# Kernel tuning notes

Measured on AMD Instinct MI355X. Metric: run time of the kernel, lower is better.

The kernel has to match this reference:

```python
import jax, jax.numpy as jnp
import numpy as np

N = 256  # node_num, fully-connected graph
NEG_SLOPE = 0.2


def _edges(n):
    # fully-connected permutations; PyG GATConv removes then re-adds self-loops,
    # so effectively all n*n (src, dst) pairs are present.
    idx = jnp.arange(n)
    src = jnp.repeat(idx, n)
    dst = jnp.tile(idx, n)
    return src, dst


def _gat_conv(x, W, att_src, att_dst, b, src, dst, n):
    # x: [N, Fin], W: [Fin, H*C], att_*: [H, C], b: [H*C]
    H, C = att_src.shape
    h = (x @ W).reshape(n, H, C)                       # [N, H, C]
    a_src = jnp.einsum('nhc,hc->nh', h, att_src)       # [N, H]
    a_dst = jnp.einsum('nhc,hc->nh', h, att_dst)
    e = jax.nn.leaky_relu(a_src[src] + a_dst[dst], NEG_SLOPE)  # [E, H]
    # segment softmax over incoming edges of each dst node
    m = jax.ops.segment_max(e, dst, num_segments=n)    # [N, H]
    p = jnp.exp(e - m[dst])
    denom = jax.ops.segment_sum(p, dst, num_segments=n)
    alpha = p / (denom[dst] + 1e-16)                   # [E, H]
    msg = h[src] * alpha[:, :, None]                   # [E, H, C]
    out = jax.ops.segment_sum(msg, dst, num_segments=n)  # [N, H, C]
    return out.reshape(n, H * C) + b


def setup_inputs() -> dict:
    key = jax.random.key(0)
    ks = jax.random.split(key, 7)
    Fin, H1, C1 = 128, 4, 128
    s = lambda fan: 1.0 / np.sqrt(fan)
    return {
        'x': jax.random.normal(ks[0], (8, N, Fin), dtype=jnp.float32),
        'W1': jax.random.normal(ks[1], (Fin, H1 * C1), dtype=jnp.float32) * s(Fin),
        'att_src1': jax.random.normal(ks[2], (H1, C1), dtype=jnp.float32) * s(C1),
        'att_dst1': jax.random.normal(ks[3], (H1, C1), dtype=jnp.float32) * s(C1),
        'b1': jnp.zeros((H1 * C1,), dtype=jnp.float32),
        'W2': jax.random.normal(ks[4], (H1 * C1, Fin), dtype=jnp.float32) * s(H1 * C1),
        'att_src2': jax.random.normal(ks[5], (1, Fin), dtype=jnp.float32) * s(Fin),
        'att_dst2': jax.random.normal(ks[6], (1, Fin), dtype=jnp.float32) * s(Fin),
        'b2': jnp.zeros((Fin,), dtype=jnp.float32),
    }


def reference(x, W1, att_src1, att_dst1, b1, W2, att_src2, att_dst2, b2):
    src, dst = _edges(N)

    def one_graph(xi):
        h = jax.nn.relu(_gat_conv(xi, W1, att_src1, att_dst1, b1, src, dst, N))
        return _gat_conv(h, W2, att_src2, att_dst2, b2, src, dst, N)

    return jax.vmap(one_graph)(x)  # [B, N, Fin]
```

## Files before the change

kernel.cpp:

```cpp
#include <hip/hip_runtime.h>
#include <hip/hip_bf16.h>

#define BATCH 8
#define NN    256
#define FIN   128
#define H1    4
#define C1    128
#define HC1   512
#define NEG_SLOPE 0.2f

__device__ __forceinline__ float lrelu(float v) {
    return v > 0.f ? v : NEG_SLOPE * v;
}

__global__ __launch_bounds__(512, 4)
void gemm1_fused(const float* __restrict__ x, const float* __restrict__ W1,
                 const float* __restrict__ as1, const float* __restrict__ ad1,
                 float* __restrict__ h1, float* __restrict__ a_src,
                 float* __restrict__ a_dst) {
    __shared__ float xs[4][FIN];
    __shared__ float redS[4][8], redD[4][8];
    const int b = blockIdx.y, r0 = blockIdx.x * 4, t = threadIdx.x;

    if (t < 128)
        ((float4*)xs)[t] = ((const float4*)(x + (size_t)(b * NN + r0) * FIN))[t];
    __syncthreads();

    float a0 = 0.f, a1 = 0.f, a2 = 0.f, a3 = 0.f;
    #pragma unroll 8
    for (int k = 0; k < FIN; ++k) {
        float w = W1[k * HC1 + t];
        a0 = fmaf(xs[0][k], w, a0);
        a1 = fmaf(xs[1][k], w, a1);
        a2 = fmaf(xs[2][k], w, a2);
        a3 = fmaf(xs[3][k], w, a3);
    }
    float acc[4] = {a0, a1, a2, a3};
    #pragma unroll
    for (int r = 0; r < 4; ++r)
        h1[(b * NN + r0 + r) * HC1 + t] = acc[r];

    const float as = as1[t], ad = ad1[t];
    const int w = t >> 6, lane = t & 63;
    #pragma unroll
    for (int r = 0; r < 4; ++r) {
        float s = acc[r] * as, d = acc[r] * ad;
        #pragma unroll
        for (int off = 32; off > 0; off >>= 1) {
            s += __shfl_down(s, off, 64);
            d += __shfl_down(d, off, 64);
        }
        if (lane == 0) { redS[r][w] = s; redD[r][w] = d; }
    }
    __syncthreads();
    if (t < 16) {
        int r = t & 3, h = t >> 2;
        a_src[(b * NN + r0 + r) * H1 + h] = redS[r][2 * h] + redS[r][2 * h + 1];
        a_dst[(b * NN + r0 + r) * H1 + h] = redD[r][2 * h] + redD[r][2 * h + 1];
    }
}

__global__ __launch_bounds__(512, 4)
void agg1_kernel(const float* __restrict__ h1, const float* __restrict__ a_src,
                 const float* __restrict__ a_dst, const float* __restrict__ b1,
                 float* __restrict__ hrelu) {
    __shared__ float s_as[NN];
    __shared__ float s_ad[16];
    __shared__ float sp[16][NN];
    __shared__ float s_den[16];

    const int b = blockIdx.z, head = blockIdx.y, d0 = blockIdx.x * 16;
    const int t = threadIdx.x;

    if (t < NN) s_as[t] = a_src[(b * NN + t) * H1 + head];
    if (t < 16) s_ad[t] = a_dst[(b * NN + d0 + t) * H1 + head];
    __syncthreads();

    const int d = t >> 5, l = t & 31;
    const float adst = s_ad[d];
    float e[8];
    float mx = -1e30f;
    #pragma unroll
    for (int i = 0; i < 8; ++i) {
        float v = lrelu(s_as[l + i * 32] + adst);
        e[i] = v;
        mx = fmaxf(mx, v);
    }
    #pragma unroll
    for (int off = 16; off > 0; off >>= 1)
        mx = fmaxf(mx, __shfl_down(mx, off, 32));
    mx = __shfl(mx, 0, 32);
    float sum = 0.f;
    #pragma unroll
    for (int i = 0; i < 8; ++i) {
        float p = __expf(e[i] - mx);
        sp[d][l + i * 32] = p;
        sum += p;
    }
    #pragma unroll
    for (int off = 16; off > 0; off >>= 1)
        sum += __shfl_down(sum, off, 32);
    if (l == 0) s_den[d] = sum + 1e-16f;
    __syncthreads();

    const int c = t & 127, g = t >> 7;
    float c0 = 0.f, c1 = 0.f, c2 = 0.f, c3 = 0.f;
    const float* hb = h1 + (size_t)(b * NN) * HC1 + head * C1 + c;
    #pragma unroll 4
    for (int src = 0; src < NN; ++src) {
        float hv = hb[(size_t)src * HC1];
        c0 = fmaf(sp[g * 4 + 0][src], hv, c0);
        c1 = fmaf(sp[g * 4 + 1][src], hv, c1);
        c2 = fmaf(sp[g * 4 + 2][src], hv, c2);
        c3 = fmaf(sp[g * 4 + 3][src], hv, c3);
    }
    float accs[4] = {c0, c1, c2, c3};
    const float bias = b1[head * C1 + c];
    #pragma unroll
    for (int j = 0; j < 4; ++j) {
        int dst = d0 + g * 4 + j;
        float v = accs[j] / s_den[g * 4 + j] + bias;
        hrelu[(b * NN + dst) * HC1 + head * C1 + c] = fmaxf(v, 0.f);
    }
}

__global__ __launch_bounds__(512, 4)
void gemm2_fused(const float* __restrict__ hrelu, const float* __restrict__ W2,
                 const float* __restrict__ as2, const float* __restrict__ ad2,
                 float* __restrict__ h2, float* __restrict__ a_src,
                 float* __restrict__ a_dst) {
    __shared__ float xs[4][HC1];
    __shared__ float red[3][4][FIN];
    __shared__ float redS[4][2], redD[4][2];
    const int b = blockIdx.y, r0 = blockIdx.x * 4, t = threadIdx.x;

    ((float4*)xs)[t] = ((const float4*)(hrelu + (size_t)(b * NN + r0) * HC1))[t];
    __syncthreads();

    const int c = t & 127, g = t >> 7;
    float acc[4] = {0.f, 0.f, 0.f, 0.f};
    const int k0 = g * 128;
    #pragma unroll 8
    for (int kk = 0; kk < 128; ++kk) {
        int k = k0 + kk;
        float w = W2[k * FIN + c];
        acc[0] = fmaf(xs[0][k], w, acc[0]);
        acc[1] = fmaf(xs[1][k], w, acc[1]);
        acc[2] = fmaf(xs[2][k], w, acc[2]);
        acc[3] = fmaf(xs[3][k], w, acc[3]);
    }
    if (g > 0) {
        #pragma unroll
        for (int r = 0; r < 4; ++r) red[g - 1][r][c] = acc[r];
    }
    __syncthreads();
    if (g == 0) {
        #pragma unroll
        for (int r = 0; r < 4; ++r) {
            acc[r] += red[0][r][c] + red[1][r][c] + red[2][r][c];
            h2[(b * NN + r0 + r) * FIN + c] = acc[r];
        }
        const int lane = t & 63, w2 = t >> 6;
        const float as = as2[c], ad = ad2[c];
        #pragma unroll
        for (int r = 0; r < 4; ++r) {
            float s = acc[r] * as, d = acc[r] * ad;
            #pragma unroll
            for (int off = 32; off > 0; off >>= 1) {
                s += __shfl_down(s, off, 64);
                d += __shfl_down(d, off, 64);
            }
            if (lane == 0) { redS[r][w2] = s; redD[r][w2] = d; }
        }
    }
    __syncthreads();
    if (t < 4) {
        a_src[b * NN + r0 + t] = redS[t][0] + redS[t][1];
        a_dst[b * NN + r0 + t] = redD[t][0] + redD[t][1];
    }
}

__global__ __launch_bounds__(512, 4)
void agg2_kernel(const float* __restrict__ h2, const float* __restrict__ a_src,
                 const float* __restrict__ a_dst, const float* __restrict__ b2,
                 float* __restrict__ out) {
    __shared__ float s_as[NN];
    __shared__ float s_ad[4];
    __shared__ float sp[4][NN];
    __shared__ float redm[4][2], reds[4][2];
    __shared__ float s_den[4];
    __shared__ float redA[3][4][FIN];

    const int b = blockIdx.y, d0 = blockIdx.x * 4, t = threadIdx.x;

    if (t < NN) s_as[t] = a_src[b * NN + t];
    if (t < 4) s_ad[t] = a_dst[b * NN + d0 + t];
    __syncthreads();

    const int d = t >> 7, l = t & 127, lane = t & 63, w = (t >> 6) & 1;
    const float adst = s_ad[d];
    float e0 = lrelu(s_as[l] + adst);
    float e1 = lrelu(s_as[l + 128] + adst);
    float mx = fmaxf(e0, e1);
    #pragma unroll
    for (int off = 32; off > 0; off >>= 1)
        mx = fmaxf(mx, __shfl_down(mx, off, 64));
    if (lane == 0) redm[d][w] = mx;
    __syncthreads();
    const float m = fmaxf(redm[d][0], redm[d][1]);
    float p0 = __expf(e0 - m), p1 = __expf(e1 - m);
    sp[d][l] = p0;
    sp[d][l + 128] = p1;
    float sum = p0 + p1;
    #pragma unroll
    for (int off = 32; off > 0; off >>= 1)
        sum += __shfl_down(sum, off, 64);
    if (lane == 0) reds[d][w] = sum;
    __syncthreads();
    if (t < 4) s_den[t] = reds[t][0] + reds[t][1] + 1e-16f;
    __syncthreads();

    const int c = l, q = d;
    float a4[4] = {0.f, 0.f, 0.f, 0.f};
    const float* hb = h2 + ((size_t)(b * NN) + q * 64) * FIN + c;
    #pragma unroll 8
    for (int i = 0; i < 64; ++i) {
        float hv = hb[(size_t)i * FIN];
        int src = q * 64 + i;
        a4[0] = fmaf(sp[0][src], hv, a4[0]);
        a4[1] = fmaf(sp[1][src], hv, a4[1]);
        a4[2] = fmaf(sp[2][src], hv, a4[2]);
        a4[3] = fmaf(sp[3][src], hv, a4[3]);
    }
    if (q > 0) {
        #pragma unroll
        for (int j = 0; j < 4; ++j) redA[q - 1][j][c] = a4[j];
    }
    __syncthreads();
    if (q == 0) {
        #pragma unroll
        for (int j = 0; j < 4; ++j) {
            float v = a4[j] + redA[0][j][c] + redA[1][j][c] + redA[2][j][c];
            out[(b * NN + d0 + j) * FIN + c] = v / s_den[j] + b2[c];
        }
    }
}

extern "C" void kernel_launch(void* const* d_in, const int* in_sizes, int n_in,
                              void* d_out, int out_size, void* d_ws, size_t ws_size,
                              hipStream_t stream) {
    const float* x   = (const float*)d_in[0];
    const float* W1  = (const float*)d_in[1];
    const float* as1 = (const float*)d_in[2];
    const float* ad1 = (const float*)d_in[3];
    const float* b1  = (const float*)d_in[4];
    const float* W2  = (const float*)d_in[5];
    const float* as2 = (const float*)d_in[6];
    const float* ad2 = (const float*)d_in[7];
    const float* b2  = (const float*)d_in[8];
    float* out = (float*)d_out;

    float* ws = (float*)d_ws;
    float* h1     = ws;
    float* hrelu  = ws + 1048576;
    float* h2     = ws + 2097152;
    float* a_src1 = ws + 2359296;
    float* a_dst1 = ws + 2367488;
    float* a_src2 = ws + 2375680;
    float* a_dst2 = ws + 2377728;

    gemm1_fused<<<dim3(64, BATCH), 512, 0, stream>>>(x, W1, as1, ad1, h1, a_src1, a_dst1);
    agg1_kernel<<<dim3(16, H1, BATCH), 512, 0, stream>>>(h1, a_src1, a_dst1, b1, hrelu);
    gemm2_fused<<<dim3(64, BATCH), 512, 0, stream>>>(hrelu, W2, as2, ad2, h2, a_src2, a_dst2);
    agg2_kernel<<<dim3(64, BATCH), 512, 0, stream>>>(h2, a_src2, a_dst2, b2, out);
}
```

Before: 122.7 us.

## Register-tile gemm1 with float4 outputs and transpose softmax weights for vector LDS reads

gemm1 now has each thread compute a 4x4 output tile from 16-row blocks of x, loading W1 as float4 and cutting the grid to 256 threads per block. This raises reuse of the W1 loads, which is meant to reduce global memory traffic. The attention-weight buffers in both aggregation kernels are stored transposed (src-major), so one float4 LDS read supplies all four destinations per step. gemm2 reads x from shared memory as float4. The trade-off is fewer blocks in gemm1, which may leave the GPU underoccupied, and extra padding in shared memory.

Result: slower. 129.1 us (+5.2%).

```diff
diff --git a/kernel.cpp b/kernel.cpp
--- a/kernel.cpp
+++ b/kernel.cpp
@@ -12,51 +12,89 @@
 __device__ __forceinline__ float lrelu(float v) {
     return v > 0.f ? v : NEG_SLOPE * v;
 }
-
-__global__ __launch_bounds__(512, 4)
+__device__ __forceinline__ float4 f4fma(float s, float4 w, float4 a) {
+    a.x = fmaf(s, w.x, a.x); a.y = fmaf(s, w.y, a.y);
+    a.z = fmaf(s, w.z, a.z); a.w = fmaf(s, w.w, a.w);
+    return a;
+}
+
+__global__ __launch_bounds__(256, 4)
 void gemm1_fused(const float* __restrict__ x, const float* __restrict__ W1,
                  const float* __restrict__ as1, const float* __restrict__ ad1,
                  float* __restrict__ h1, float* __restrict__ a_src,
                  float* __restrict__ a_dst) {
-    __shared__ float xs[4][FIN];
-    __shared__ float redS[4][8], redD[4][8];
-    const int b = blockIdx.y, r0 = blockIdx.x * 4, t = threadIdx.x;
-
-    if (t < 128)
-        ((float4*)xs)[t] = ((const float4*)(x + (size_t)(b * NN + r0) * FIN))[t];
-    __syncthreads();
-
-    float a0 = 0.f, a1 = 0.f, a2 = 0.f, a3 = 0.f;
-    #pragma unroll 8
-    for (int k = 0; k < FIN; ++k) {
-        float w = W1[k * HC1 + t];
-        a0 = fmaf(xs[0][k], w, a0);
-        a1 = fmaf(xs[1][k], w, a1);
-        a2 = fmaf(xs[2][k], w, a2);
-        a3 = fmaf(xs[3][k], w, a3);
-    }
-    float acc[4] = {a0, a1, a2, a3};
-    #pragma unroll
-    for (int r = 0; r < 4; ++r)
-        h1[(b * NN + r0 + r) * HC1 + t] = acc[r];
-
-    const float as = as1[t], ad = ad1[t];
-    const int w = t >> 6, lane = t & 63;
-    #pragma unroll
-    for (int r = 0; r < 4; ++r) {
-        float s = acc[r] * as, d = acc[r] * ad;
-        #pragma unroll
-        for (int off = 32; off > 0; off >>= 1) {
-            s += __shfl_down(s, off, 64);
-            d += __shfl_down(d, off, 64);
+    __shared__ float xs[16][FIN];
+    __shared__ float redS[4][2][4], redD[4][2][4];
+    const int bx = blockIdx.x, b = blockIdx.y, t = threadIdx.x;
+    const int rt = bx & 15, ch = bx >> 4;
+    const int q = t & 63, rg = t >> 6;
+
+    {
+        const float4* xp = (const float4*)(x + ((size_t)b * NN + rt * 16) * FIN);
+        float4* x4 = (float4*)xs;
+        x4[t] = xp[t];
+        x4[t + 256] = xp[t + 256];
+    }
+    __syncthreads();
+
+    const int col0 = ch * 256 + q * 4;
+    float4 a0 = {0,0,0,0}, a1 = {0,0,0,0}, a2 = {0,0,0,0}, a3 = {0,0,0,0};
+    const float4* xr0 = (const float4*)&xs[rg * 4 + 0][0];
+    const float4* xr1 = (const float4*)&xs[rg * 4 + 1][0];
+    const float4* xr2 = (const float4*)&xs[rg * 4 + 2][0];
+    const float4* xr3 = (const float4*)&xs[rg * 4 + 3][0];
+    #pragma unroll 4
+    for (int kq = 0; kq < 32; ++kq) {
+        float4 x0 = xr0[kq], x1 = xr1[kq], x2 = xr2[kq], x3 = xr3[kq];
+        const float* wb = W1 + (size_t)(kq * 4) * HC1 + col0;
+        float4 w0 = *(const float4*)(wb);
+        float4 w1 = *(const float4*)(wb + HC1);
+        float4 w2 = *(const float4*)(wb + 2 * HC1);
+        float4 w3 = *(const float4*)(wb + 3 * HC1);
+        a0 = f4fma(x0.x, w0, a0); a0 = f4fma(x0.y, w1, a0);
+        a0 = f4fma(x0.z, w2, a0); a0 = f4fma(x0.w, w3, a0);
+        a1 = f4fma(x1.x, w0, a1); a1 = f4fma(x1.y, w1, a1);
+        a1 = f4fma(x1.z, w2, a1); a1 = f4fma(x1.w, w3, a1);
+        a2 = f4fma(x2.x, w0, a2); a2 = f4fma(x2.y, w1, a2);
+        a2 = f4fma(x2.z, w2, a2); a2 = f4fma(x2.w, w3, a2);
+        a3 = f4fma(x3.x, w0, a3); a3 = f4fma(x3.y, w1, a3);
+        a3 = f4fma(x3.z, w2, a3); a3 = f4fma(x3.w, w3, a3);
+    }
+
+    const size_t rowbase = (size_t)b * NN + rt * 16 + rg * 4;
+    *(float4*)(h1 + (rowbase + 0) * HC1 + col0) = a0;
+    *(float4*)(h1 + (rowbase + 1) * HC1 + col0) = a1;
+    *(float4*)(h1 + (rowbase + 2) * HC1 + col0) = a2;
+    *(float4*)(h1 + (rowbase + 3) * HC1 + col0) = a3;
+
+    float4 asv = *(const float4*)(as1 + col0);
+    float4 adv = *(const float4*)(ad1 + col0);
+    float s[4], d[4];
+    float4 accs[4] = {a0, a1, a2, a3};
+    #pragma unroll
+    for (int i = 0; i < 4; ++i) {
+        s[i] = accs[i].x * asv.x + accs[i].y * asv.y + accs[i].z * asv.z + accs[i].w * asv.w;
+        d[i] = accs[i].x * adv.x + accs[i].y * adv.y + accs[i].z * adv.z + accs[i].w * adv.w;
+    }
+    #pragma unroll
+    for (int off = 16; off > 0; off >>= 1) {
+        #pragma unroll
+        for (int i = 0; i < 4; ++i) {
+            s[i] += __shfl_down(s[i], off, 32);
+            d[i] += __shfl_down(d[i], off, 32);
         }
-        if (lane == 0) { redS[r][w] = s; redD[r][w] = d; }
-    }
-    __syncthreads();
-    if (t < 16) {
-        int r = t & 3, h = t >> 2;
-        a_src[(b * NN + r0 + r) * H1 + h] = redS[r][2 * h] + redS[r][2 * h + 1];
-        a_dst[(b * NN + r0 + r) * H1 + h] = redD[r][2 * h] + redD[r][2 * h + 1];
+    }
+    if ((t & 31) == 0) {
+        int hh = q >> 5;
+        #pragma unroll
+        for (int i = 0; i < 4; ++i) { redS[rg][hh][i] = s[i]; redD[rg][hh][i] = d[i]; }
+    }
+    __syncthreads();
+    if (t < 32) {
+        int rg2 = t >> 3, hh = (t >> 2) & 1, r = t & 3;
+        size_t node = (size_t)b * NN + rt * 16 + rg2 * 4 + r;
+        a_src[node * H1 + ch * 2 + hh] = redS[rg2][hh][r];
+        a_dst[node * H1 + ch * 2 + hh] = redD[rg2][hh][r];
     }
 }
 
@@ -66,7 +104,7 @@
                  float* __restrict__ hrelu) {
     __shared__ float s_as[NN];
     __shared__ float s_ad[16];
-    __shared__ float sp[16][NN];
+    __shared__ float spT[NN][20];
     __shared__ float s_den[16];
 
     const int b = blockIdx.z, head = blockIdx.y, d0 = blockIdx.x * 16;
@@ -94,7 +132,7 @@
     #pragma unroll
     for (int i = 0; i < 8; ++i) {
         float p = __expf(e[i] - mx);
-        sp[d][l + i * 32] = p;
+        spT[l + i * 32][d] = p;
         sum += p;
     }
     #pragma unroll
@@ -109,10 +147,11 @@
     #pragma unroll 4
     for (int src = 0; src < NN; ++src) {
         float hv = hb[(size_t)src * HC1];
-        c0 = fmaf(sp[g * 4 + 0][src], hv, c0);
-        c1 = fmaf(sp[g * 4 + 1][src], hv, c1);
-        c2 = fmaf(sp[g * 4 + 2][src], hv, c2);
-        c3 = fmaf(sp[g * 4 + 3][src], hv, c3);
+        float4 p4 = *(const float4*)&spT[src][g * 4];
+        c0 = fmaf(p4.x, hv, c0);
+        c1 = fmaf(p4.y, hv, c1);
+        c2 = fmaf(p4.z, hv, c2);
+        c3 = fmaf(p4.w, hv, c3);
     }
     float accs[4] = {c0, c1, c2, c3};
     const float bias = b1[head * C1 + c];
@@ -139,15 +178,26 @@
 
     const int c = t & 127, g = t >> 7;
     float acc[4] = {0.f, 0.f, 0.f, 0.f};
-    const int k0 = g * 128;
-    #pragma unroll 8
-    for (int kk = 0; kk < 128; ++kk) {
-        int k = k0 + kk;
-        float w = W2[k * FIN + c];
-        acc[0] = fmaf(xs[0][k], w, acc[0]);
-        acc[1] = fmaf(xs[1][k], w, acc[1]);
-        acc[2] = fmaf(xs[2][k], w, acc[2]);
-        acc[3] = fmaf(xs[3][k], w, acc[3]);
+    const float4* x40 = (const float4*)&xs[0][g * 128];
+    const float4* x41 = (const float4*)&xs[1][g * 128];
+    const float4* x42 = (const float4*)&xs[2][g * 128];
+    const float4* x43 = (const float4*)&xs[3][g * 128];
+    const float* wb = W2 + (size_t)(g * 128) * FIN + c;
+    #pragma unroll 4
+    for (int kq = 0; kq < 32; ++kq) {
+        float4 x0 = x40[kq], x1 = x41[kq], x2 = x42[kq], x3 = x43[kq];
+        float w0 = wb[(size_t)(kq * 4 + 0) * FIN];
+        float w1 = wb[(size_t)(kq * 4 + 1) * FIN];
+        float w2 = wb[(size_t)(kq * 4 + 2) * FIN];
+        float w3 = wb[(size_t)(kq * 4 + 3) * FIN];
+        acc[0] = fmaf(x0.x, w0, acc[0]); acc[0] = fmaf(x0.y, w1, acc[0]);
+        acc[0] = fmaf(x0.z, w2, acc[0]); acc[0] = fmaf(x0.w, w3, acc[0]);
+        acc[1] = fmaf(x1.x, w0, acc[1]); acc[1] = fmaf(x1.y, w1, acc[1]);
+        acc[1] = fmaf(x1.z, w2, acc[1]); acc[1] = fmaf(x1.w, w3, acc[1]);
+        acc[2] = fmaf(x2.x, w0, acc[2]); acc[2] = fmaf(x2.y, w1, acc[2]);
+        acc[2] = fmaf(x2.z, w2, acc[2]); acc[2] = fmaf(x2.w, w3, acc[2]);
+        acc[3] = fmaf(x3.x, w0, acc[3]); acc[3] = fmaf(x3.y, w1, acc[3]);
+        acc[3] = fmaf(x3.z, w2, acc[3]); acc[3] = fmaf(x3.w, w3, acc[3]);
     }
     if (g > 0) {
         #pragma unroll
@@ -160,17 +210,17 @@
             acc[r] += red[0][r][c] + red[1][r][c] + red[2][r][c];
             h2[(b * NN + r0 + r) * FIN + c] = acc[r];
         }
-        const int lane = t & 63, w2 = t >> 6;
+        const int lane = t & 63, w2v = t >> 6;
         const float as = as2[c], ad = ad2[c];
         #pragma unroll
         for (int r = 0; r < 4; ++r) {
-            float s = acc[r] * as, d = acc[r] * ad;
+            float s = acc[r] * as, dd = acc[r] * ad;
             #pragma unroll
             for (int off = 32; off > 0; off >>= 1) {
                 s += __shfl_down(s, off, 64);
-                d += __shfl_down(d, off, 64);
+                dd += __shfl_down(dd, off, 64);
             }
-            if (lane == 0) { redS[r][w2] = s; redD[r][w2] = d; }
+            if (lane == 0) { redS[r][w2v] = s; redD[r][w2v] = dd; }
         }
     }
     __syncthreads();
@@ -186,7 +236,7 @@
                  float* __restrict__ out) {
     __shared__ float s_as[NN];
     __shared__ float s_ad[4];
-    __shared__ float sp[4][NN];
+    __shared__ float spT[NN][8];
     __shared__ float redm[4][2], reds[4][2];
     __shared__ float s_den[4];
     __shared__ float redA[3][4][FIN];
@@ -209,8 +259,8 @@
     __syncthreads();
     const float m = fmaxf(redm[d][0], redm[d][1]);
     float p0 = __expf(e0 - m), p1 = __expf(e1 - m);
-    sp[d][l] = p0;
-    sp[d][l + 128] = p1;
+    spT[l][d] = p0;
+    spT[l + 128][d] = p1;
     float sum = p0 + p1;
     #pragma unroll
     for (int off = 32; off > 0; off >>= 1)
@@ -223,14 +273,14 @@
     const int c = l, q = d;
     float a4[4] = {0.f, 0.f, 0.f, 0.f};
     const float* hb = h2 + ((size_t)(b * NN) + q * 64) * FIN + c;
-    #pragma unroll 8
+    #pragma unroll 4
     for (int i = 0; i < 64; ++i) {
         float hv = hb[(size_t)i * FIN];
-        int src = q * 64 + i;
-        a4[0] = fmaf(sp[0][src], hv, a4[0]);
-        a4[1] = fmaf(sp[1][src], hv, a4[1]);
-        a4[2] = fmaf(sp[2][src], hv, a4[2]);
-        a4[3] = fmaf(sp[3][src], hv, a4[3]);
+        float4 p4 = *(const float4*)&spT[q * 64 + i][0];
+        a4[0] = fmaf(p4.x, hv, a4[0]);
+        a4[1] = fmaf(p4.y, hv, a4[1]);
+        a4[2] = fmaf(p4.z, hv, a4[2]);
+        a4[3] = fmaf(p4.w, hv, a4[3]);
     }
     if (q > 0) {
         #pragma unroll
@@ -269,7 +319,7 @@
     float* a_src2 = ws + 2375680;
     float* a_dst2 = ws + 2377728;
 
-    gemm1_fused<<<dim3(64, BATCH), 512, 0, stream>>>(x, W1, as1, ad1, h1, a_src1, a_dst1);
+    gemm1_fused<<<dim3(32, BATCH), 256, 0, stream>>>(x, W1, as1, ad1, h1, a_src1, a_dst1);
     agg1_kernel<<<dim3(16, H1, BATCH), 512, 0, stream>>>(h1, a_src1, a_dst1, b1, hrelu);
     gemm2_fused<<<dim3(64, BATCH), 512, 0, stream>>>(hrelu, W2, as2, ad2, h2, a_src2, a_dst2);
     agg2_kernel<<<dim3(64, BATCH), 512, 0, stream>>>(h2, a_src2, a_dst2, b2, out);
```

## Fuse layer-1 aggregation with layer-2 GEMM via shared-memory intermediate

Applied to the files above, without the earlier changes.

Merges the first attention aggregation and the second linear projection into one kernel that keeps the ReLU'd hidden rows in shared memory, removing a global write/read of the intermediate and one kernel launch. Each block now processes 8 destination nodes across all heads with transposed softmax weights for vector loads, raising reuse of h1 and W2 loads. In exchange, the grid halves and shared memory per block grows large, which limits occupancy.

After: 117.7 us. 1.04x faster.

```diff
diff --git a/kernel.cpp b/kernel.cpp
--- a/kernel.cpp
+++ b/kernel.cpp
@@ -60,123 +60,136 @@
     }
 }
 
-__global__ __launch_bounds__(512, 4)
-void agg1_kernel(const float* __restrict__ h1, const float* __restrict__ a_src,
-                 const float* __restrict__ a_dst, const float* __restrict__ b1,
-                 float* __restrict__ hrelu) {
-    __shared__ float s_as[NN];
-    __shared__ float s_ad[16];
-    __shared__ float sp[16][NN];
-    __shared__ float s_den[16];
-
-    const int b = blockIdx.z, head = blockIdx.y, d0 = blockIdx.x * 16;
-    const int t = threadIdx.x;
-
-    if (t < NN) s_as[t] = a_src[(b * NN + t) * H1 + head];
-    if (t < 16) s_ad[t] = a_dst[(b * NN + d0 + t) * H1 + head];
-    __syncthreads();
-
-    const int d = t >> 5, l = t & 31;
-    const float adst = s_ad[d];
-    float e[8];
-    float mx = -1e30f;
-    #pragma unroll
-    for (int i = 0; i < 8; ++i) {
-        float v = lrelu(s_as[l + i * 32] + adst);
-        e[i] = v;
-        mx = fmaxf(mx, v);
-    }
-    #pragma unroll
-    for (int off = 16; off > 0; off >>= 1)
-        mx = fmaxf(mx, __shfl_down(mx, off, 32));
-    mx = __shfl(mx, 0, 32);
-    float sum = 0.f;
-    #pragma unroll
-    for (int i = 0; i < 8; ++i) {
-        float p = __expf(e[i] - mx);
-        sp[d][l + i * 32] = p;
-        sum += p;
-    }
-    #pragma unroll
-    for (int off = 16; off > 0; off >>= 1)
-        sum += __shfl_down(sum, off, 32);
-    if (l == 0) s_den[d] = sum + 1e-16f;
-    __syncthreads();
-
-    const int c = t & 127, g = t >> 7;
-    float c0 = 0.f, c1 = 0.f, c2 = 0.f, c3 = 0.f;
-    const float* hb = h1 + (size_t)(b * NN) * HC1 + head * C1 + c;
-    #pragma unroll 4
-    for (int src = 0; src < NN; ++src) {
-        float hv = hb[(size_t)src * HC1];
-        c0 = fmaf(sp[g * 4 + 0][src], hv, c0);
-        c1 = fmaf(sp[g * 4 + 1][src], hv, c1);
-        c2 = fmaf(sp[g * 4 + 2][src], hv, c2);
-        c3 = fmaf(sp[g * 4 + 3][src], hv, c3);
-    }
-    float accs[4] = {c0, c1, c2, c3};
-    const float bias = b1[head * C1 + c];
-    #pragma unroll
-    for (int j = 0; j < 4; ++j) {
-        int dst = d0 + g * 4 + j;
-        float v = accs[j] / s_den[g * 4 + j] + bias;
-        hrelu[(b * NN + dst) * HC1 + head * C1 + c] = fmaxf(v, 0.f);
-    }
-}
-
-__global__ __launch_bounds__(512, 4)
-void gemm2_fused(const float* __restrict__ hrelu, const float* __restrict__ W2,
-                 const float* __restrict__ as2, const float* __restrict__ ad2,
-                 float* __restrict__ h2, float* __restrict__ a_src,
-                 float* __restrict__ a_dst) {
-    __shared__ float xs[4][HC1];
-    __shared__ float red[3][4][FIN];
-    __shared__ float redS[4][2], redD[4][2];
-    const int b = blockIdx.y, r0 = blockIdx.x * 4, t = threadIdx.x;
-
-    ((float4*)xs)[t] = ((const float4*)(hrelu + (size_t)(b * NN + r0) * HC1))[t];
-    __syncthreads();
-
-    const int c = t & 127, g = t >> 7;
-    float acc[4] = {0.f, 0.f, 0.f, 0.f};
-    const int k0 = g * 128;
-    #pragma unroll 8
-    for (int kk = 0; kk < 128; ++kk) {
-        int k = k0 + kk;
-        float w = W2[k * FIN + c];
-        acc[0] = fmaf(xs[0][k], w, acc[0]);
-        acc[1] = fmaf(xs[1][k], w, acc[1]);
-        acc[2] = fmaf(xs[2][k], w, acc[2]);
-        acc[3] = fmaf(xs[3][k], w, acc[3]);
+__global__ __launch_bounds__(512, 2)
+void mid_fused(const float* __restrict__ h1, const float* __restrict__ a_src,
+               const float* __restrict__ a_dst, const float* __restrict__ b1,
+               const float* __restrict__ W2, const float* __restrict__ as2,
+               const float* __restrict__ ad2, float* __restrict__ h2,
+               float* __restrict__ a_src2, float* __restrict__ a_dst2) {
+    __shared__ __align__(16) float s_as[H1][NN];
+    __shared__ float s_ad[H1][8];
+    __shared__ __align__(16) float spT[NN][36];
+    __shared__ float s_den[32];
+    __shared__ __align__(16) float hrelu_s[8][HC1];
+    __shared__ float red[3][8][FIN];
+    __shared__ float redS[8][2], redD[8][2];
+
+    const int b = blockIdx.y, d0 = blockIdx.x * 8, t = threadIdx.x;
+
+    {
+        int i0 = t, i1 = t + 512;
+        ((float*)s_as)[ (i0 >> 8) * NN + (i0 & 255) ] = a_src[(b * NN + (i0 & 255)) * H1 + (i0 >> 8)];
+        ((float*)s_as)[ (i1 >> 8) * NN + (i1 & 255) ] = a_src[(b * NN + (i1 & 255)) * H1 + (i1 >> 8)];
+        if (t < 32) {
+            int h = t >> 3, d = t & 7;
+            s_ad[h][d] = a_dst[(b * NN + d0 + d) * H1 + h];
+        }
+    }
+    __syncthreads();
+
+    {
+        const int pair = t >> 4, sub = t & 15;
+        const int h = pair >> 3, d = pair & 7;
+        const float adst = s_ad[h][d];
+        float e[16];
+        float mx = -1e30f;
+        #pragma unroll
+        for (int i = 0; i < 16; ++i) {
+            float v = lrelu(s_as[h][sub + i * 16] + adst);
+            e[i] = v;
+            mx = fmaxf(mx, v);
+        }
+        #pragma unroll
+        for (int off = 8; off > 0; off >>= 1)
+            mx = fmaxf(mx, __shfl_down(mx, off, 16));
+        mx = __shfl(mx, 0, 16);
+        float sum = 0.f;
+        #pragma unroll
+        for (int i = 0; i < 16; ++i) {
+            float p = __expf(e[i] - mx);
+            spT[sub + i * 16][pair] = p;
+            sum += p;
+        }
+        #pragma unroll
+        for (int off = 8; off > 0; off >>= 1)
+            sum += __shfl_down(sum, off, 16);
+        if (sub == 0) s_den[pair] = sum + 1e-16f;
+    }
+    __syncthreads();
+
+    {
+        const int ct = t, h = t >> 7;
+        float acc8[8] = {0,0,0,0,0,0,0,0};
+        const float* hb = h1 + (size_t)(b * NN) * HC1 + ct;
+        #pragma unroll 4
+        for (int src = 0; src < NN; ++src) {
+            float hv = hb[(size_t)src * HC1];
+            float4 pa = *(const float4*)&spT[src][h * 8];
+            float4 pb = *(const float4*)&spT[src][h * 8 + 4];
+            acc8[0] = fmaf(pa.x, hv, acc8[0]);
+            acc8[1] = fmaf(pa.y, hv, acc8[1]);
+            acc8[2] = fmaf(pa.z, hv, acc8[2]);
+            acc8[3] = fmaf(pa.w, hv, acc8[3]);
+            acc8[4] = fmaf(pb.x, hv, acc8[4]);
+            acc8[5] = fmaf(pb.y, hv, acc8[5]);
+            acc8[6] = fmaf(pb.z, hv, acc8[6]);
+            acc8[7] = fmaf(pb.w, hv, acc8[7]);
+        }
+        const float bias = b1[ct];
+        #pragma unroll
+        for (int d = 0; d < 8; ++d)
+            hrelu_s[d][ct] = fmaxf(acc8[d] / s_den[h * 8 + d] + bias, 0.f);
+    }
+    __syncthreads();
+
+    const int c2 = t & 127, g = t >> 7;
+    float acc[8] = {0,0,0,0,0,0,0,0};
+    {
+        const float* wb = W2 + (size_t)(g * 128) * FIN + c2;
+        #pragma unroll 2
+        for (int kq = 0; kq < 32; ++kq) {
+            float w0 = wb[(size_t)(kq * 4 + 0) * FIN];
+            float w1 = wb[(size_t)(kq * 4 + 1) * FIN];
+            float w2 = wb[(size_t)(kq * 4 + 2) * FIN];
+            float w3 = wb[(size_t)(kq * 4 + 3) * FIN];
+            #pragma unroll
+            for (int r = 0; r < 8; ++r) {
+                float4 xv = *(const float4*)&hrelu_s[r][g * 128 + kq * 4];
+                acc[r] = fmaf(xv.x, w0, acc[r]);
+                acc[r] = fmaf(xv.y, w1, acc[r]);
+                acc[r] = fmaf(xv.z, w2, acc[r]);
+                acc[r] = fmaf(xv.w, w3, acc[r]);
+            }
+        }
     }
     if (g > 0) {
         #pragma unroll
-        for (int r = 0; r < 4; ++r) red[g - 1][r][c] = acc[r];
+        for (int r = 0; r < 8; ++r) red[g - 1][r][c2] = acc[r];
     }
     __syncthreads();
     if (g == 0) {
         #pragma unroll
-        for (int r = 0; r < 4; ++r) {
-            acc[r] += red[0][r][c] + red[1][r][c] + red[2][r][c];
-            h2[(b * NN + r0 + r) * FIN + c] = acc[r];
-        }
-        const int lane = t & 63, w2 = t >> 6;
-        const float as = as2[c], ad = ad2[c];
-        #pragma unroll
-        for (int r = 0; r < 4; ++r) {
-            float s = acc[r] * as, d = acc[r] * ad;
+        for (int r = 0; r < 8; ++r) {
+            acc[r] += red[0][r][c2] + red[1][r][c2] + red[2][r][c2];
+            h2[(b * NN + d0 + r) * FIN + c2] = acc[r];
+        }
+        const int lane = t & 63, wv = t >> 6;
+        const float as = as2[c2], ad = ad2[c2];
+        #pragma unroll
+        for (int r = 0; r < 8; ++r) {
+            float s = acc[r] * as, dd = acc[r] * ad;
             #pragma unroll
             for (int off = 32; off > 0; off >>= 1) {
                 s += __shfl_down(s, off, 64);
-                d += __shfl_down(d, off, 64);
+                dd += __shfl_down(dd, off, 64);
             }
-            if (lane == 0) { redS[r][w2] = s; redD[r][w2] = d; }
-        }
-    }
-    __syncthreads();
-    if (t < 4) {
-        a_src[b * NN + r0 + t] = redS[t][0] + redS[t][1];
-        a_dst[b * NN + r0 + t] = redD[t][0] + redD[t][1];
+            if (lane == 0) { redS[r][wv] = s; redD[r][wv] = dd; }
+        }
+    }
+    __syncthreads();
+    if (t < 8) {
+        a_src2[b * NN + d0 + t] = redS[t][0] + redS[t][1];
+        a_dst2[b * NN + d0 + t] = redD[t][0] + redD[t][1];
     }
 }
 
@@ -262,15 +275,14 @@
 
     float* ws = (float*)d_ws;
     float* h1     = ws;
-    float* hrelu  = ws + 1048576;
-    float* h2     = ws + 2097152;
-    float* a_src1 = ws + 2359296;
-    float* a_dst1 = ws + 2367488;
-    float* a_src2 = ws + 2375680;
-    float* a_dst2 = ws + 2377728;
+    float* h2     = ws + 1048576;
+    float* a_src1 = ws + 1310720;
+    float* a_dst1 = ws + 1318912;
+    float* a_src2 = ws + 1327104;
+    float* a_dst2 = ws + 1329152;
 
     gemm1_fused<<<dim3(64, BATCH), 512, 0, stream>>>(x, W1, as1, ad1, h1, a_src1, a_dst1);
-    agg1_kernel<<<dim3(16, H1, BATCH), 512, 0, stream>>>(h1, a_src1, a_dst1, b1, hrelu);
-    gemm2_fused<<<dim3(64, BATCH), 512, 0, stream>>>(hrelu, W2, as2, ad2, h2, a_src2, a_dst2);
+    mid_fused<<<dim3(32, BATCH), 512, 0, stream>>>(h1, a_src1, a_dst1, b1, W2, as2, ad2,
+                                                   h2, a_src2, a_dst2);
     agg2_kernel<<<dim3(64, BATCH), 512, 0, stream>>>(h2, a_src2, a_dst2, b2, out);
 }
```
